# Kernel tuning notes

Measured on AMD Instinct MI355X. Metric: run time of the kernel, lower is better.

Reference implementation:

```python
import jax, jax.numpy as jnp
import numpy as np

BETA = 0.9      # membrane decay
THRESH = 1.0    # firing threshold


def _lif(x):
    """Leaky integrate-and-fire over leading time axis. x: (T, ..., C) -> spikes (T, ..., C)."""
    def step(mem, xt):
        mem = BETA * mem + xt
        s = (mem > THRESH).astype(xt.dtype)
        mem = mem - s * THRESH  # soft reset
        return mem, s
    _, spikes = jax.lax.scan(step, jnp.zeros_like(x[0]), x)
    return spikes


def setup_inputs() -> dict:
    key = jax.random.key(0)
    k1, k2, k3, k4, k5 = jax.random.split(key, 5)
    T, N, D = 4, 8192, 1024
    E, EF, TOPK = 8, 512, 2  # expert_ff = d_ff // n_experts = 4096 // 8
    x = jax.random.normal(k1, (T, N, D), dtype=jnp.float32)
    expert_indices = jax.random.randint(k2, (N, TOPK), 0, E)
    expert_weights = jax.random.uniform(k3, (N, TOPK), dtype=jnp.float32)
    up_w = jax.random.normal(k4, (E, EF, D), dtype=jnp.float32) * 0.02   # Linear(d_model, ef).weight
    down_w = jax.random.normal(k5, (E, D, EF), dtype=jnp.float32) * 0.02  # Linear(ef, d_model).weight
    return {"x": x, "expert_indices": expert_indices, "expert_weights": expert_weights,
            "up_w": up_w, "down_w": down_w}


def reference(x, expert_indices, expert_weights, up_w, down_w):
    T, N, D = x.shape
    E = up_w.shape[0]
    # Dense combine weights W[n, e] = sum_k weights[n, k] * (indices[n, k] == e)
    W = jnp.zeros((N, E), dtype=x.dtype).at[
        jnp.arange(N)[:, None], expert_indices].add(expert_weights)
    out = jnp.zeros_like(x)
    for e in range(E):  # fixed small loop over experts
        h = _lif(jnp.einsum('tnd,fd->tnf', x, up_w[e]))   # up-proj + LIF hidden
        o = _lif(jnp.einsum('tnf,df->tnd', h, down_w[e]))  # down-proj + LIF output
        out = out + o * W[:, e][None, :, None]             # weighted combine (0 for inactive)
    return out
```

## Files before the change

kernel.cpp:

```cpp
#include <hip/hip_runtime.h>
#include <stdint.h>

#define T_STEPS 4
#define NTOK    8192
#define DMODEL  1024
#define NEXP    8
#define EFF     512
#define BMT     128
#define CAPTOT  (2*NTOK + NEXP*BMT)

typedef __attribute__((ext_vector_type(8))) short bf8_t;
typedef __attribute__((ext_vector_type(4))) float f32x4;

#define MFMA(a,b,c) __builtin_amdgcn_mfma_f32_16x16x32_bf16((a),(b),(c),0,0,0)

#define SWZC(r, c)  ((((c) ^ (((r) >> 1) & 3))) * 8)
#define SWZ64(r, c) ((((c) ^ ((r) & 7))) * 8)

typedef __attribute__((address_space(3))) unsigned int lds_uint;
typedef const __attribute__((address_space(1))) unsigned int glb_uint;
__device__ __forceinline__ void dma16(const void* g, void* l) {
    __builtin_amdgcn_global_load_lds((glb_uint*)g, (lds_uint*)l, 16, 0, 0);
}
#define S_BARRIER() __builtin_amdgcn_s_barrier()
#define SFENCE()    __builtin_amdgcn_sched_barrier(0)

__device__ __forceinline__ int bal_tile(int bx, int n_used) {
    const int xcd = bx & 7, pos = bx >> 3;
    const int q = n_used >> 3, rr = n_used & 7;
    const int alloc = q + (xcd < rr ? 1 : 0);
    if (pos >= alloc) return n_used;
    const int base = (xcd < rr) ? xcd * (q + 1) : rr * (q + 1) + (xcd - rr) * q;
    return base + pos;
}


__device__ __forceinline__ unsigned short bf16rn(float f) {
    unsigned u = __float_as_uint(f);
    unsigned r = u + 0x7fffu + ((u >> 16) & 1u);
    return (unsigned short)(r >> 16);
}
__device__ __forceinline__ float bf2f(unsigned short h) {
    return __uint_as_float(((unsigned)h) << 16);
}
__device__ __forceinline__ unsigned pk(unsigned short a, unsigned short b) {
    return (unsigned)a | ((unsigned)b << 16);
}

__device__ __forceinline__ void split8v(float4 va, float4 vb,
                                        unsigned short* d0, unsigned short* d1,
                                        unsigned short* d2) {
    float v[8];
    *(float4*)&v[0] = va;
    *(float4*)&v[4] = vb;
    unsigned short h[8], m[8], l[8];
#pragma unroll
    for (int i = 0; i < 8; ++i) {
        unsigned short a = bf16rn(v[i]);
        float r1 = v[i] - bf2f(a);
        unsigned short b = bf16rn(r1);
        float r2 = r1 - bf2f(b);
        h[i] = a; m[i] = b; l[i] = bf16rn(r2);
    }
    *(uint4*)d0 = make_uint4(pk(h[0],h[1]), pk(h[2],h[3]), pk(h[4],h[5]), pk(h[6],h[7]));
    *(uint4*)d1 = make_uint4(pk(m[0],m[1]), pk(m[2],m[3]), pk(m[4],m[5]), pk(m[6],m[7]));
    *(uint4*)d2 = make_uint4(pk(l[0],l[1]), pk(l[2],l[3]), pk(l[4],l[5]), pk(l[6],l[7]));
}

__device__ __forceinline__ void stage8_3limb(const float* __restrict__ src,
                                             unsigned short* d0, unsigned short* d1,
                                             unsigned short* d2) {
    float4 va = *(const float4*)(src + 0);
    float4 vb = *(const float4*)(src + 4);
    split8v(va, vb, d0, d1, d2);
}


__global__ void k_split(const float* __restrict__ w, unsigned short* __restrict__ h,
                        unsigned short* __restrict__ m, unsigned short* __restrict__ l) {
    size_t i = (size_t)(blockIdx.x * blockDim.x + threadIdx.x) * 8;
    stage8_3limb(w + i, h + i, m + i, l + i);
}


__global__ void k_count(const int* __restrict__ idx, int* __restrict__ counts) {
    int n = blockIdx.x * blockDim.x + threadIdx.x;
    if (n >= NTOK) return;
    int e0 = idx[2*n], e1 = idx[2*n+1];
    atomicAdd(&counts[e0], 1);
    if (e1 != e0) atomicAdd(&counts[e1], 1);
}

__global__ void k_prefix(const int* __restrict__ counts, int* __restrict__ offsets) {
    if (threadIdx.x == 0) {
        int o = 0;
        for (int e = 0; e < NEXP; ++e) {
            offsets[e] = o;
            o += (counts[e] + BMT - 1) / BMT * BMT;
        }
        offsets[NEXP] = o;
    }
}

__global__ void k_fill(const int* __restrict__ idx, const float* __restrict__ wts,
                       const int* __restrict__ offsets, int* __restrict__ cursors,
                       int* __restrict__ tok, float* __restrict__ wgt) {
    int n = blockIdx.x * blockDim.x + threadIdx.x;
    if (n >= NTOK) return;
    int e0 = idx[2*n], e1 = idx[2*n+1];
    float w0 = wts[2*n], w1 = wts[2*n+1];
    if (e0 == e1) w0 = __fadd_rn(w0, w1);
    int p0 = offsets[e0] + atomicAdd(&cursors[e0], 1);
    tok[p0] = n; wgt[p0] = w0;
    if (e1 != e0) {
        int p1 = offsets[e1] + atomicAdd(&cursors[e1], 1);
        tok[p1] = n; wgt[p1] = w1;
    }
}


__global__ __launch_bounds__(256, 2)
void k_up(const float* __restrict__ x,
          const unsigned short* __restrict__ uwh, const unsigned short* __restrict__ uwm,
          const unsigned short* __restrict__ uwl,
          const int* __restrict__ offsets, const int* __restrict__ tok,
          unsigned short* __restrict__ spk) {
    const int n_used = offsets[NEXP] / BMT;
    const int m0 = bal_tile(blockIdx.x, n_used) * BMT;
    const int ft = blockIdx.y;
    if (m0 >= offsets[NEXP]) return;
    int e = 0;
    for (int i = 1; i < NEXP; ++i) if (m0 >= offsets[i]) e = i;

    __shared__ __align__(16) unsigned short As[3][128][32];
    __shared__ __align__(16) unsigned short Bs[2][3][128][32];

    const int tid  = threadIdx.x;
    const int lane = tid & 63, wid = tid >> 6;
    const int quad = lane >> 4, l16 = lane & 15;
    const int mw = (wid & 1) * 64, nw = (wid >> 1) * 64;

    const int r = tid >> 1, half = tid & 1;
    const int c0 = SWZC(r, half*2 + 0);
    const int c1 = SWZC(r, half*2 + 1);
    const int tokA = tok[m0 + r];
    const float* xbase = x + (size_t)tokA * DMODEL + half * 16;

    const unsigned short* wlimb[3] = { uwh, uwm, uwl };
    const size_t wrow0 = ((size_t)e * EFF + ft * 128) * DMODEL;
    const int drow  = lane >> 2;
    const int dclog = (lane & 3) ^ ((lane >> 3) & 3);

    const int kq = SWZC(l16, quad);

    f32x4 mem[4][4];
#pragma unroll
    for (int i = 0; i < 4; ++i)
#pragma unroll
        for (int j = 0; j < 4; ++j) mem[i][j] = (f32x4){0.f,0.f,0.f,0.f};

#pragma unroll
    for (int j = 0; j < 6; ++j) {
        const int limb = j >> 1, rh = j & 1;
        dma16(wlimb[limb] + wrow0 + (size_t)(rh*64 + wid*16 + drow) * DMODEL + dclog*8,
              &Bs[0][limb][rh*64 + wid*16][0]);
    }
    float4 pa[4];
#pragma unroll
    for (int i = 0; i < 4; ++i) pa[i] = ((const float4*)xbase)[i];

    int cur = 0;
    for (int t = 0; t < T_STEPS; ++t) {
        f32x4 acc[4][4];
#pragma unroll
        for (int i = 0; i < 4; ++i)
#pragma unroll
            for (int j = 0; j < 4; ++j) acc[i][j] = (f32x4){0.f,0.f,0.f,0.f};

        const float* xrow = xbase + (size_t)t * NTOK * DMODEL;

        for (int kc = 0; kc < DMODEL; kc += 32) {
            const bool last = (t == T_STEPS - 1) && (kc == DMODEL - 32);
            asm volatile("s_waitcnt lgkmcnt(0)" ::: "memory");
            SFENCE();
            S_BARRIER();
            SFENCE();
            if (!last) {
                const int nkk = (kc == DMODEL - 32) ? 0 : kc + 32;
#pragma unroll
                for (int j = 0; j < 6; ++j) {
                    const int limb = j >> 1, rh = j & 1;
                    dma16(wlimb[limb] + wrow0 + (size_t)(rh*64 + wid*16 + drow) * DMODEL
                              + nkk + dclog*8,
                          &Bs[cur ^ 1][limb][rh*64 + wid*16][0]);
                }
            }
            split8v(pa[0], pa[1], &As[0][r][c0], &As[1][r][c0], &As[2][r][c0]);
            split8v(pa[2], pa[3], &As[0][r][c1], &As[1][r][c1], &As[2][r][c1]);
            if (!last) {
                const float* nxtA = (kc == DMODEL - 32)
                    ? xbase + (size_t)(t + 1) * NTOK * DMODEL
                    : xrow + kc + 32;
#pragma unroll
                for (int i = 0; i < 4; ++i) pa[i] = ((const float4*)nxtA)[i];
                asm volatile("s_waitcnt vmcnt(10) lgkmcnt(0)" ::: "memory");
            } else {
                asm volatile("s_waitcnt vmcnt(0) lgkmcnt(0)" ::: "memory");
            }
            SFENCE();
            S_BARRIER();
            SFENCE();

            bf8_t bh[4], bm[4], bl[4];
#pragma unroll
            for (int nt = 0; nt < 4; ++nt) {
                const int nr = nw + nt*16 + l16;
                bh[nt] = *(const bf8_t*)&Bs[cur][0][nr][kq];
                bm[nt] = *(const bf8_t*)&Bs[cur][1][nr][kq];
                bl[nt] = *(const bf8_t*)&Bs[cur][2][nr][kq];
            }
#pragma unroll
            for (int mt = 0; mt < 4; ++mt) {
                const int mr = mw + mt*16 + l16;
                bf8_t ah = *(const bf8_t*)&As[0][mr][kq];
                bf8_t am = *(const bf8_t*)&As[1][mr][kq];
                bf8_t al = *(const bf8_t*)&As[2][mr][kq];
#pragma unroll
                for (int nt = 0; nt < 4; ++nt) {
                    f32x4 c = acc[mt][nt];
                    c = MFMA(ah, bh[nt], c);
                    c = MFMA(am, bh[nt], c);
                    c = MFMA(ah, bm[nt], c);
                    c = MFMA(am, bm[nt], c);
                    c = MFMA(al, bh[nt], c);
                    c = MFMA(ah, bl[nt], c);
                    acc[mt][nt] = c;
                }
            }
            cur ^= 1;
        }

#pragma unroll
        for (int mt = 0; mt < 4; ++mt)
#pragma unroll
            for (int nt = 0; nt < 4; ++nt)
#pragma unroll
                for (int reg = 0; reg < 4; ++reg) {
                    float mv = __fadd_rn(__fmul_rn(0.9f, mem[mt][nt][reg]), acc[mt][nt][reg]);
                    bool s = mv > 1.0f;
                    mem[mt][nt][reg] = __fsub_rn(mv, s ? 1.0f : 0.0f);
                    int row = m0 + mw + mt*16 + quad*4 + reg;
                    int col = ft*128 + nw + nt*16 + l16;
                    spk[((size_t)t * CAPTOT + row) * EFF + col] = s ? 0x3F80u : 0u;
                }
    }
}


__global__ __launch_bounds__(256, 2)
void k_dn(const unsigned short* __restrict__ spk,
          const unsigned short* __restrict__ dwh, const unsigned short* __restrict__ dwm,
          const unsigned short* __restrict__ dwl,
          const int* __restrict__ offsets, const int* __restrict__ tok,
          const float* __restrict__ wgt, float* __restrict__ out) {
    const int n_used = offsets[NEXP] / BMT;
    const int m0 = bal_tile(blockIdx.x, n_used) * BMT;
    const int dt = blockIdx.y;
    if (m0 >= offsets[NEXP]) return;
    int e = 0;
    for (int i = 1; i < NEXP; ++i) if (m0 >= offsets[i]) e = i;

    __shared__ __align__(16) unsigned short As[2][128][64];
    __shared__ __align__(16) unsigned short Bs[3][128][64];

    const int tid  = threadIdx.x;
    const int lane = tid & 63, wid = tid >> 6;
    const int quad = lane >> 4, l16 = lane & 15;
    const int mw = (wid & 1) * 64, nw = (wid >> 1) * 64;

    const unsigned short* dlimb[3] = { dwh, dwm, dwl };
    const size_t drow0 = ((size_t)e * DMODEL + dt * 128) * EFF;
    const int drow8 = lane >> 3;
    const int dclog = (lane & 7) ^ ((lane >> 3) & 7);

    f32x4 mem[4][4];
#pragma unroll
    for (int i = 0; i < 4; ++i)
#pragma unroll
        for (int j = 0; j < 4; ++j) mem[i][j] = (f32x4){0.f,0.f,0.f,0.f};

#pragma unroll
    for (int j2 = 0; j2 < 4; ++j2) {
        const int rowb = wid*32 + j2*8;
        dma16(spk + ((size_t)(m0 + rowb + drow8)) * EFF + dclog*8,
              &As[0][rowb][0]);
    }

    int cur = 0;
    for (int t = 0; t < T_STEPS; ++t) {
        f32x4 acc[4][4];
#pragma unroll
        for (int i = 0; i < 4; ++i)
#pragma unroll
            for (int j = 0; j < 4; ++j) acc[i][j] = (f32x4){0.f,0.f,0.f,0.f};

        for (int kc = 0; kc < EFF; kc += 64) {
            const bool last = (t == T_STEPS - 1) && (kc == EFF - 64);
            asm volatile("s_waitcnt lgkmcnt(0)" ::: "memory");
            SFENCE();
            S_BARRIER();
            SFENCE();
#pragma unroll
            for (int limb = 0; limb < 3; ++limb)
#pragma unroll
                for (int j2 = 0; j2 < 4; ++j2) {
                    const int rowb = wid*32 + j2*8;
                    dma16(dlimb[limb] + drow0 + (size_t)(rowb + drow8) * EFF + kc + dclog*8,
                          &Bs[limb][rowb][0]);
                }
            if (!last) {
                int ntt = t, nkk = kc + 64;
                if (nkk == EFF) { nkk = 0; ntt = t + 1; }
#pragma unroll
                for (int j2 = 0; j2 < 4; ++j2) {
                    const int rowb = wid*32 + j2*8;
                    dma16(spk + ((size_t)ntt * CAPTOT + m0 + rowb + drow8) * EFF + nkk + dclog*8,
                          &As[cur ^ 1][rowb][0]);
                }
                asm volatile("s_waitcnt vmcnt(4)" ::: "memory");
            } else {
                asm volatile("s_waitcnt vmcnt(0)" ::: "memory");
            }
            SFENCE();
            S_BARRIER();
            SFENCE();

#pragma unroll
            for (int kk = 0; kk < 2; ++kk) {
                bf8_t bh[4], bm[4], bl[4];
#pragma unroll
                for (int nt = 0; nt < 4; ++nt) {
                    const int nr = nw + nt*16 + l16;
                    const int kb = SWZ64(nr, quad + kk*4);
                    bh[nt] = *(const bf8_t*)&Bs[0][nr][kb];
                    bm[nt] = *(const bf8_t*)&Bs[1][nr][kb];
                    bl[nt] = *(const bf8_t*)&Bs[2][nr][kb];
                }
#pragma unroll
                for (int mt = 0; mt < 4; ++mt) {
                    const int mr = mw + mt*16 + l16;
                    bf8_t a = *(const bf8_t*)&As[cur][mr][SWZ64(mr, quad + kk*4)];
#pragma unroll
                    for (int nt = 0; nt < 4; ++nt) {
                        f32x4 c = acc[mt][nt];
                        c = MFMA(a, bh[nt], c);
                        c = MFMA(a, bm[nt], c);
                        c = MFMA(a, bl[nt], c);
                        acc[mt][nt] = c;
                    }
                }
            }
            cur ^= 1;
        }

#pragma unroll
        for (int mt = 0; mt < 4; ++mt) {
            const int rbase = m0 + mw + mt*16 + quad*4;
#pragma unroll
            for (int reg = 0; reg < 4; ++reg) {
                const int   n = tok[rbase + reg];
                const float w = wgt[rbase + reg];
#pragma unroll
                for (int nt = 0; nt < 4; ++nt) {
                    float mv = __fadd_rn(__fmul_rn(0.9f, mem[mt][nt][reg]), acc[mt][nt][reg]);
                    bool s = mv > 1.0f;
                    mem[mt][nt][reg] = __fsub_rn(mv, s ? 1.0f : 0.0f);
                    if (s && w != 0.0f) {
                        int col = dt*128 + nw + nt*16 + l16;
                        atomicAdd(out + ((size_t)t * NTOK + n) * DMODEL + col, w);
                    }
                }
            }
        }
    }
}


extern "C" void kernel_launch(void* const* d_in, const int* in_sizes, int n_in,
                              void* d_out, int out_size, void* d_ws, size_t ws_size,
                              hipStream_t stream) {
    const float* x      = (const float*)d_in[0];
    const int*   idx    = (const int*)  d_in[1];
    const float* wts    = (const float*)d_in[2];
    const float* up_w   = (const float*)d_in[3];
    const float* down_w = (const float*)d_in[4];
    float* out = (float*)d_out;

    char* ws = (char*)d_ws;
    int*   counts  = (int*)(ws + 0);
    int*   cursors = (int*)(ws + 32);
    int*   offsets = (int*)(ws + 64);
    int*   tok     = (int*)(ws + 128);
    float* wgt     = (float*)(ws + 128 + (size_t)CAPTOT * 4);
    unsigned short* spk = (unsigned short*)(ws + 128 + (size_t)CAPTOT * 8);

    const size_t WSPK = (size_t)T_STEPS * CAPTOT * EFF * 2;
    size_t base2 = 128 + (size_t)CAPTOT * 8 + WSPK;
    base2 = (base2 + 511) & ~(size_t)511;
    const size_t WLIMB = (size_t)NEXP * EFF * DMODEL * 2;
    unsigned short* uwh = (unsigned short*)(ws + base2);
    unsigned short* uwm = (unsigned short*)(ws + base2 + 1*WLIMB);
    unsigned short* uwl = (unsigned short*)(ws + base2 + 2*WLIMB);
    unsigned short* dwh = (unsigned short*)(ws + base2 + 3*WLIMB);
    unsigned short* dwm = (unsigned short*)(ws + base2 + 4*WLIMB);
    unsigned short* dwl = (unsigned short*)(ws + base2 + 5*WLIMB);

    hipMemsetAsync(ws, 0, 128 + (size_t)CAPTOT * 8, stream);
    hipMemsetAsync(out, 0, (size_t)out_size * sizeof(float), stream);

    const int nsplit = NEXP * EFF * DMODEL / 8 / 256;
    k_split<<<nsplit, 256, 0, stream>>>(up_w,   uwh, uwm, uwl);
    k_split<<<nsplit, 256, 0, stream>>>(down_w, dwh, dwm, dwl);

    k_count <<<(NTOK + 255) / 256, 256, 0, stream>>>(idx, counts);
    k_prefix<<<1, 64, 0, stream>>>(counts, offsets);
    k_fill  <<<(NTOK + 255) / 256, 256, 0, stream>>>(idx, wts, offsets, cursors, tok, wgt);

    dim3 gup(CAPTOT / BMT, EFF / 128);
    k_up<<<gup, 256, 0, stream>>>(x, uwh, uwm, uwl, offsets, tok, spk);

    dim3 gdn(CAPTOT / BMT, DMODEL / 128);
    k_dn<<<gdn, 256, 0, stream>>>(spk, dwh, dwm, dwl, offsets, tok, wgt, out);
}
```

Before: 903.9 us.

## Double-buffer weight limbs in k_dn, use 512 threads, packed bf16 split conversion

The down-projection kernel now double-buffers the three bf16 weight limbs in LDS alongside the spike tile, so the weight loads for the next k-chunk overlap the current MFMA work instead of being waited on each iteration. The block grows from 256 to 512 threads (8 waves), and each wave covers a 64x32 output sub-tile instead of 64x64, halving accumulator registers per wave. The weight split kernel switches from manual bit-twiddling bf16 rounding to the packed HIP float2-to-bfloat162 conversion intrinsic. The cost is doubled LDS for the B tiles, which may limit occupancy, plus more waves contending at each barrier.

```diff
diff --git a/kernel.cpp b/kernel.cpp
--- a/kernel.cpp
+++ b/kernel.cpp
@@ -1,4 +1,5 @@
 #include <hip/hip_runtime.h>
+#include <hip/hip_bf16.h>
 #include <stdint.h>
 
 #define T_STEPS 4
@@ -35,16 +36,17 @@
 }
 
 
-__device__ __forceinline__ unsigned short bf16rn(float f) {
-    unsigned u = __float_as_uint(f);
-    unsigned r = u + 0x7fffu + ((u >> 16) & 1u);
-    return (unsigned short)(r >> 16);
-}
-__device__ __forceinline__ float bf2f(unsigned short h) {
-    return __uint_as_float(((unsigned)h) << 16);
-}
-__device__ __forceinline__ unsigned pk(unsigned short a, unsigned short b) {
-    return (unsigned)a | ((unsigned)b << 16);
+__device__ __forceinline__ unsigned cvtpk2(float a, float b, float& ra, float& rb) {
+    __hip_bfloat162 h = __float22bfloat162_rn(make_float2(a, b));
+    union { __hip_bfloat162 h2; unsigned u; } cv; cv.h2 = h;
+    ra = a - __bfloat162float(h.x);
+    rb = b - __bfloat162float(h.y);
+    return cv.u;
+}
+__device__ __forceinline__ unsigned cvtpk2f(float a, float b) {
+    union { __hip_bfloat162 h2; unsigned u; } cv;
+    cv.h2 = __float22bfloat162_rn(make_float2(a, b));
+    return cv.u;
 }
 
 __device__ __forceinline__ void split8v(float4 va, float4 vb,
@@ -53,18 +55,17 @@
     float v[8];
     *(float4*)&v[0] = va;
     *(float4*)&v[4] = vb;
-    unsigned short h[8], m[8], l[8];
-#pragma unroll
-    for (int i = 0; i < 8; ++i) {
-        unsigned short a = bf16rn(v[i]);
-        float r1 = v[i] - bf2f(a);
-        unsigned short b = bf16rn(r1);
-        float r2 = r1 - bf2f(b);
-        h[i] = a; m[i] = b; l[i] = bf16rn(r2);
-    }
-    *(uint4*)d0 = make_uint4(pk(h[0],h[1]), pk(h[2],h[3]), pk(h[4],h[5]), pk(h[6],h[7]));
-    *(uint4*)d1 = make_uint4(pk(m[0],m[1]), pk(m[2],m[3]), pk(m[4],m[5]), pk(m[6],m[7]));
-    *(uint4*)d2 = make_uint4(pk(l[0],l[1]), pk(l[2],l[3]), pk(l[4],l[5]), pk(l[6],l[7]));
+    unsigned hw[4], mw[4], lw[4];
+#pragma unroll
+    for (int p = 0; p < 4; ++p) {
+        float r0, r1, s0, s1;
+        hw[p] = cvtpk2(v[2*p], v[2*p+1], r0, r1);
+        mw[p] = cvtpk2(r0, r1, s0, s1);
+        lw[p] = cvtpk2f(s0, s1);
+    }
+    *(uint4*)d0 = make_uint4(hw[0], hw[1], hw[2], hw[3]);
+    *(uint4*)d1 = make_uint4(mw[0], mw[1], mw[2], mw[3]);
+    *(uint4*)d2 = make_uint4(lw[0], lw[1], lw[2], lw[3]);
 }
 
 __device__ __forceinline__ void stage8_3limb(const float* __restrict__ src,
@@ -257,7 +258,7 @@
 }
 
 
-__global__ __launch_bounds__(256, 2)
+__global__ __launch_bounds__(512, 2)
 void k_dn(const unsigned short* __restrict__ spk,
           const unsigned short* __restrict__ dwh, const unsigned short* __restrict__ dwm,
           const unsigned short* __restrict__ dwl,
@@ -271,38 +272,41 @@
     for (int i = 1; i < NEXP; ++i) if (m0 >= offsets[i]) e = i;
 
     __shared__ __align__(16) unsigned short As[2][128][64];
-    __shared__ __align__(16) unsigned short Bs[3][128][64];
+    __shared__ __align__(16) unsigned short Bs[2][3][128][64];
 
     const int tid  = threadIdx.x;
     const int lane = tid & 63, wid = tid >> 6;
     const int quad = lane >> 4, l16 = lane & 15;
-    const int mw = (wid & 1) * 64, nw = (wid >> 1) * 64;
+    const int mw = (wid & 1) * 64, nw = (wid >> 1) * 32;
 
     const unsigned short* dlimb[3] = { dwh, dwm, dwl };
     const size_t drow0 = ((size_t)e * DMODEL + dt * 128) * EFF;
     const int drow8 = lane >> 3;
     const int dclog = (lane & 7) ^ ((lane >> 3) & 7);
 
-    f32x4 mem[4][4];
-#pragma unroll
-    for (int i = 0; i < 4; ++i)
-#pragma unroll
-        for (int j = 0; j < 4; ++j) mem[i][j] = (f32x4){0.f,0.f,0.f,0.f};
-
-#pragma unroll
-    for (int j2 = 0; j2 < 4; ++j2) {
-        const int rowb = wid*32 + j2*8;
-        dma16(spk + ((size_t)(m0 + rowb + drow8)) * EFF + dclog*8,
-              &As[0][rowb][0]);
-    }
+    f32x4 mem[4][2];
+#pragma unroll
+    for (int i = 0; i < 4; ++i) { mem[i][0] = (f32x4){0.f,0.f,0.f,0.f}; mem[i][1] = (f32x4){0.f,0.f,0.f,0.f}; }
+
+#pragma unroll
+    for (int j2 = 0; j2 < 2; ++j2) {
+        const int rowb = wid*16 + j2*8;
+        dma16(spk + ((size_t)(m0 + rowb + drow8)) * EFF + dclog*8, &As[0][rowb][0]);
+    }
+#pragma unroll
+    for (int limb = 0; limb < 3; ++limb)
+#pragma unroll
+        for (int j2 = 0; j2 < 2; ++j2) {
+            const int rowb = wid*16 + j2*8;
+            dma16(dlimb[limb] + drow0 + (size_t)(rowb + drow8) * EFF + dclog*8,
+                  &Bs[0][limb][rowb][0]);
+        }
 
     int cur = 0;
     for (int t = 0; t < T_STEPS; ++t) {
-        f32x4 acc[4][4];
-#pragma unroll
-        for (int i = 0; i < 4; ++i)
-#pragma unroll
-            for (int j = 0; j < 4; ++j) acc[i][j] = (f32x4){0.f,0.f,0.f,0.f};
+        f32x4 acc[4][2];
+#pragma unroll
+        for (int i = 0; i < 4; ++i) { acc[i][0] = (f32x4){0.f,0.f,0.f,0.f}; acc[i][1] = (f32x4){0.f,0.f,0.f,0.f}; }
 
         for (int kc = 0; kc < EFF; kc += 64) {
             const bool last = (t == T_STEPS - 1) && (kc == EFF - 64);
@@ -310,24 +314,24 @@
             SFENCE();
             S_BARRIER();
             SFENCE();
-#pragma unroll
-            for (int limb = 0; limb < 3; ++limb)
-#pragma unroll
-                for (int j2 = 0; j2 < 4; ++j2) {
-                    const int rowb = wid*32 + j2*8;
-                    dma16(dlimb[limb] + drow0 + (size_t)(rowb + drow8) * EFF + kc + dclog*8,
-                          &Bs[limb][rowb][0]);
-                }
             if (!last) {
                 int ntt = t, nkk = kc + 64;
                 if (nkk == EFF) { nkk = 0; ntt = t + 1; }
 #pragma unroll
-                for (int j2 = 0; j2 < 4; ++j2) {
-                    const int rowb = wid*32 + j2*8;
+                for (int j2 = 0; j2 < 2; ++j2) {
+                    const int rowb = wid*16 + j2*8;
                     dma16(spk + ((size_t)ntt * CAPTOT + m0 + rowb + drow8) * EFF + nkk + dclog*8,
                           &As[cur ^ 1][rowb][0]);
                 }
-                asm volatile("s_waitcnt vmcnt(4)" ::: "memory");
+#pragma unroll
+                for (int limb = 0; limb < 3; ++limb)
+#pragma unroll
+                    for (int j2 = 0; j2 < 2; ++j2) {
+                        const int rowb = wid*16 + j2*8;
+                        dma16(dlimb[limb] + drow0 + (size_t)(rowb + drow8) * EFF + nkk + dclog*8,
+                              &Bs[cur ^ 1][limb][rowb][0]);
+                    }
+                asm volatile("s_waitcnt vmcnt(8)" ::: "memory");
             } else {
                 asm volatile("s_waitcnt vmcnt(0)" ::: "memory");
             }
@@ -337,21 +341,21 @@
 
 #pragma unroll
             for (int kk = 0; kk < 2; ++kk) {
-                bf8_t bh[4], bm[4], bl[4];
-#pragma unroll
-                for (int nt = 0; nt < 4; ++nt) {
+                bf8_t bh[2], bm[2], bl[2];
+#pragma unroll
+                for (int nt = 0; nt < 2; ++nt) {
                     const int nr = nw + nt*16 + l16;
                     const int kb = SWZ64(nr, quad + kk*4);
-                    bh[nt] = *(const bf8_t*)&Bs[0][nr][kb];
-                    bm[nt] = *(const bf8_t*)&Bs[1][nr][kb];
-                    bl[nt] = *(const bf8_t*)&Bs[2][nr][kb];
+                    bh[nt] = *(const bf8_t*)&Bs[cur][0][nr][kb];
+                    bm[nt] = *(const bf8_t*)&Bs[cur][1][nr][kb];
+                    bl[nt] = *(const bf8_t*)&Bs[cur][2][nr][kb];
                 }
 #pragma unroll
                 for (int mt = 0; mt < 4; ++mt) {
                     const int mr = mw + mt*16 + l16;
                     bf8_t a = *(const bf8_t*)&As[cur][mr][SWZ64(mr, quad + kk*4)];
 #pragma unroll
-                    for (int nt = 0; nt < 4; ++nt) {
+                    for (int nt = 0; nt < 2; ++nt) {
                         f32x4 c = acc[mt][nt];
                         c = MFMA(a, bh[nt], c);
                         c = MFMA(a, bm[nt], c);
@@ -371,7 +375,7 @@
                 const int   n = tok[rbase + reg];
                 const float w = wgt[rbase + reg];
 #pragma unroll
-                for (int nt = 0; nt < 4; ++nt) {
+                for (int nt = 0; nt < 2; ++nt) {
                     float mv = __fadd_rn(__fmul_rn(0.9f, mem[mt][nt][reg]), acc[mt][nt][reg]);
                     bool s = mv > 1.0f;
                     mem[mt][nt][reg] = __fsub_rn(mv, s ? 1.0f : 0.0f);
@@ -430,5 +434,5 @@
     k_up<<<gup, 256, 0, stream>>>(x, uwh, uwm, uwl, offsets, tok, spk);
 
     dim3 gdn(CAPTOT / BMT, DMODEL / 128);
-    k_dn<<<gdn, 256, 0, stream>>>(spk, dwh, dwm, dwl, offsets, tok, wgt, out);
-}
+    k_dn<<<gdn, 512, 0, stream>>>(spk, dwh, dwm, dwl, offsets, tok, wgt, out);
+}
```

After: 943.6 us. 4.4% more time.
